# Optimization experiments

Measured on AMD Instinct MI355X. Metric: run time of the kernel, lower is better.

The kernel has to match this reference:

```python
import jax, jax.numpy as jnp
import numpy as np

VLAD_K = 8   # vlad_cluster
GHOST_K = 2  # ghost_cluster
IN_DIM = 512
EPS = 1e-12  # F.normalize eps


def setup_inputs() -> dict:
    key = jax.random.key(0)
    k1, k2, k3, k4 = jax.random.split(key, 4)
    N, C, H, W = 32, IN_DIM, 16, 64
    KG = VLAD_K + GHOST_K
    x = jax.random.normal(k1, (N, C, H, W), dtype=jnp.float32)
    # 1x1 conv weight [KG, C, 1, 1] -> store as [KG, C]; bias [KG]
    conv_w = jax.random.normal(k2, (KG, C), dtype=jnp.float32) * (1.0 / np.sqrt(C))
    conv_b = jax.random.normal(k3, (KG,), dtype=jnp.float32) * 0.01
    centers = jax.random.uniform(k4, (KG, C), dtype=jnp.float32)
    return {"x": x, "conv_w": conv_w, "conv_b": conv_b, "centers": centers}


def reference(x, conv_w, conv_b, centers):
    N, C, H, W = x.shape
    P = H * W
    xf = x.reshape(N, C, P)                                   # [N,C,P]
    # 1x1 conv == per-position matmul over channels
    logits = jnp.einsum('ncp,kc->nkp', xf, conv_w) + conv_b[None, :, None]
    a = jax.nn.softmax(logits, axis=1)                        # softmax over clusters, [N,KG,P]
    # algebraic rewrite of sum_p a*(x - c): (a @ x^T) - (sum_p a) * c
    ax = jnp.einsum('nkp,ncp->nkc', a, xf)                    # [N,KG,C]
    a_sum = a.sum(axis=-1)                                    # [N,KG]
    cluster_res = ax - a_sum[..., None] * centers[None]       # [N,KG,C]
    cluster_res = cluster_res[:, :VLAD_K, :]                  # drop ghost clusters
    norm = jnp.linalg.norm(cluster_res, axis=-1, keepdims=True)
    cluster_res = cluster_res / jnp.maximum(norm, EPS)        # L2 normalize per cluster
    return cluster_res.reshape(N, VLAD_K * C)
```

## Files before the change

### kernel.cpp

```cpp
#include <hip/hip_runtime.h>
#include <math.h>

#define N_    32
#define C_    512
#define P_    1024
#define KG_   10
#define KV_   8
#define PBLK_ 64
#define NPB_  (P_ / PBLK_)
#define PS_   81

__global__ __launch_bounds__(512) void vlad_logits(
    const float* __restrict__ x, const float* __restrict__ w,
    const float* __restrict__ bias, float* __restrict__ a_ws,
    float* __restrict__ asum_blk) {
  __shared__ float part[PBLK_ * PS_];
  const int t  = threadIdx.x;
  const int pl = t & 63;
  const int cg = __builtin_amdgcn_readfirstlane(threadIdx.x >> 6);
  const int n  = blockIdx.x >> 4;
  const int pb = blockIdx.x & 15;
  const int p0 = pb * PBLK_;

  const float* xp = x + ((size_t)n * C_ + cg * 64) * P_ + p0 + pl;

  float acc[KG_];
#pragma unroll
  for (int k = 0; k < KG_; ++k) acc[k] = 0.f;

#pragma unroll 8
  for (int i = 0; i < 64; ++i) {
    const float xv = xp[(size_t)i * P_];
    const int c = cg * 64 + i;
#pragma unroll
    for (int k = 0; k < KG_; ++k) acc[k] += xv * w[k * C_ + c];
  }

#pragma unroll
  for (int k = 0; k < KG_; ++k) part[pl * PS_ + cg * KG_ + k] = acc[k];
  __syncthreads();

  if (t < 64) {
    float l[KG_];
    float m = -1e30f;
#pragma unroll
    for (int k = 0; k < KG_; ++k) {
      float s = bias[k];
#pragma unroll
      for (int g = 0; g < 8; ++g) s += part[t * PS_ + g * KG_ + k];
      l[k] = s;
      m = fmaxf(m, s);
    }
    float sum = 0.f;
#pragma unroll
    for (int k = 0; k < KG_; ++k) { l[k] = __expf(l[k] - m); sum += l[k]; }
    const float inv = 1.f / sum;
#pragma unroll
    for (int k = 0; k < KV_; ++k) {
      const float a = l[k] * inv;
      a_ws[((size_t)n * KV_ + k) * P_ + p0 + t] = a;
      float s = a;
      s += __shfl_xor(s, 1, 64);  s += __shfl_xor(s, 2, 64);
      s += __shfl_xor(s, 4, 64);  s += __shfl_xor(s, 8, 64);
      s += __shfl_xor(s, 16, 64); s += __shfl_xor(s, 32, 64);
      if (t == 0) asum_blk[(n * NPB_ + pb) * KV_ + k] = s;
    }
  }
}

__global__ __launch_bounds__(256) void vlad_ax(
    const float* __restrict__ x, const float* __restrict__ a_ws,
    float* __restrict__ ax_ws) {
  const int n    = blockIdx.x >> 5;
  const int cb   = blockIdx.x & 31;
  const int lane = threadIdx.x & 63;
  const int wv   = threadIdx.x >> 6;
  const int c0   = cb * 16 + wv * 4;

  const float* ap = a_ws + (size_t)n * KV_ * P_;
  const float* xp = x + (size_t)n * C_ * P_;

  float acc[4][8];
#pragma unroll
  for (int cc = 0; cc < 4; ++cc)
#pragma unroll
    for (int k = 0; k < 8; ++k) acc[cc][k] = 0.f;

#pragma unroll
  for (int i = 0; i < 4; ++i) {
    const int pb = i * 256 + lane * 4;
    float4 a4[8];
#pragma unroll
    for (int k = 0; k < 8; ++k)
      a4[k] = *reinterpret_cast<const float4*>(ap + (size_t)k * P_ + pb);
#pragma unroll
    for (int cc = 0; cc < 4; ++cc) {
      float4 x4 = *reinterpret_cast<const float4*>(xp + (size_t)(c0 + cc) * P_ + pb);
#pragma unroll
      for (int k = 0; k < 8; ++k)
        acc[cc][k] += x4.x * a4[k].x + x4.y * a4[k].y
                    + x4.z * a4[k].z + x4.w * a4[k].w;
    }
  }

  float v[32];
#pragma unroll
  for (int cc = 0; cc < 4; ++cc)
#pragma unroll
    for (int k = 0; k < 8; ++k) v[cc * 8 + k] = acc[cc][k];

  {
    const bool hi = lane & 1;
#pragma unroll
    for (int j = 0; j < 16; ++j) {
      float send = hi ? v[j] : v[j + 16];
      float keep = hi ? v[j + 16] : v[j];
      v[j] = keep + __shfl_xor(send, 1, 64);
    }
  }
  {
    const bool hi = lane & 2;
#pragma unroll
    for (int j = 0; j < 8; ++j) {
      float send = hi ? v[j] : v[j + 8];
      float keep = hi ? v[j + 8] : v[j];
      v[j] = keep + __shfl_xor(send, 2, 64);
    }
  }
  {
    const bool hi = lane & 4;
#pragma unroll
    for (int j = 0; j < 4; ++j) {
      float send = hi ? v[j] : v[j + 4];
      float keep = hi ? v[j + 4] : v[j];
      v[j] = keep + __shfl_xor(send, 4, 64);
    }
  }
  {
    const bool hi = lane & 8;
#pragma unroll
    for (int j = 0; j < 2; ++j) {
      float send = hi ? v[j] : v[j + 2];
      float keep = hi ? v[j + 2] : v[j];
      v[j] = keep + __shfl_xor(send, 8, 64);
    }
  }
  {
    const bool hi = lane & 16;
    float send = hi ? v[0] : v[1];
    float keep = hi ? v[1] : v[0];
    v[0] = keep + __shfl_xor(send, 16, 64);
  }
  v[0] += __shfl_xor(v[0], 32, 64);

  if (lane < 32) {
    const int o = ((lane & 1) << 4) | ((lane & 2) << 2) | (lane & 4)
                | (((lane >> 3) & 1) << 1) | ((lane >> 4) & 1);
    const int cc = o >> 3;
    const int k  = o & 7;
    ax_ws[((size_t)n * KV_ + k) * C_ + (c0 + cc)] = v[0];
  }
}

__global__ __launch_bounds__(256) void vlad_fin(
    const float* __restrict__ ax_ws, const float* __restrict__ asum_blk,
    const float* __restrict__ centers, float* __restrict__ out) {
  __shared__ float sred[4];
  const int n = blockIdx.x >> 3;
  const int k = blockIdx.x & 7;
  const int t = threadIdx.x, lane = t & 63, wv = t >> 6;

  float asv = 0.f;
#pragma unroll
  for (int pb = 0; pb < NPB_; ++pb)
    asv += asum_blk[(n * NPB_ + pb) * KV_ + k];

  const int c = t * 2;
  const float2 av = *reinterpret_cast<const float2*>(&ax_ws[((size_t)n * KV_ + k) * C_ + c]);
  const float2 ct = *reinterpret_cast<const float2*>(&centers[k * C_ + c]);
  const float r0 = av.x - asv * ct.x;
  const float r1 = av.y - asv * ct.y;

  float ss = r0 * r0 + r1 * r1;
#pragma unroll
  for (int d = 1; d < 64; d <<= 1) ss += __shfl_xor(ss, d, 64);
  if (lane == 0) sred[wv] = ss;
  __syncthreads();
  const float tot = (sred[0] + sred[1]) + (sred[2] + sred[3]);
  const float inv = 1.f / fmaxf(sqrtf(tot), 1e-12f);

  out[(size_t)n * (KV_ * C_) + k * C_ + c]     = r0 * inv;
  out[(size_t)n * (KV_ * C_) + k * C_ + c + 1] = r1 * inv;
}

extern "C" void kernel_launch(void* const* d_in, const int* in_sizes, int n_in,
                              void* d_out, int out_size, void* d_ws, size_t ws_size,
                              hipStream_t stream) {
  const float* x       = (const float*)d_in[0];
  const float* conv_w  = (const float*)d_in[1];
  const float* conv_b  = (const float*)d_in[2];
  const float* centers = (const float*)d_in[3];
  float* out = (float*)d_out;

  float* a_ws     = (float*)d_ws;
  float* ax_ws    = a_ws + (size_t)N_ * KV_ * P_;
  float* asum_blk = ax_ws + (size_t)N_ * KV_ * C_;

  hipLaunchKernelGGL(vlad_logits, dim3(N_ * NPB_), dim3(512), 0, stream,
                     x, conv_w, conv_b, a_ws, asum_blk);
  hipLaunchKernelGGL(vlad_ax,     dim3(N_ * 32),   dim3(256), 0, stream,
                     x, a_ws, ax_ws);
  hipLaunchKernelGGL(vlad_fin,    dim3(N_ * KV_),  dim3(256), 0, stream,
                     ax_ws, asum_blk, centers, out);
}
```

Before: 116.2 us.

## Split channel and position reductions across more blocks with separate softmax kernel

The logits kernel now splits the channel reduction into two halves per position block, doubling the grid to 1024 blocks and writing partial logits to workspace. A new small softmax kernel combines the two partials, applies bias and softmax, and produces the assignments and per-block sums. The ax kernel likewise splits positions into two halves for twice as many blocks, and the final kernel adds the two partial ax results. The aim is more parallelism on a GPU with many CUs, at the cost of an extra kernel launch and extra workspace traffic.

```diff
diff --git a/kernel.cpp b/kernel.cpp
--- a/kernel.cpp
+++ b/kernel.cpp
@@ -10,75 +10,95 @@
 #define NPB_  (P_ / PBLK_)
 #define PS_   81
 
-__global__ __launch_bounds__(512) void vlad_logits(
+__global__ __launch_bounds__(512, 8) void vlad_logits_p(
     const float* __restrict__ x, const float* __restrict__ w,
-    const float* __restrict__ bias, float* __restrict__ a_ws,
-    float* __restrict__ asum_blk) {
+    float* __restrict__ plg) {
   __shared__ float part[PBLK_ * PS_];
   const int t  = threadIdx.x;
   const int pl = t & 63;
-  const int cg = __builtin_amdgcn_readfirstlane(threadIdx.x >> 6);
+  const int cg = __builtin_amdgcn_readfirstlane(t >> 6);
+  const int bx = blockIdx.x;
+  const int n  = bx >> 5;
+  const int pb = (bx >> 1) & 15;
+  const int ch = bx & 1;
+  const int p0 = pb * PBLK_;
+  const int c0 = ch * 256 + cg * 32;
+
+  const float* xp = x + ((size_t)n * C_ + c0) * P_ + p0 + pl;
+  const float* wp = w + c0;
+
+  float acc[KG_];
+#pragma unroll
+  for (int k = 0; k < KG_; ++k) acc[k] = 0.f;
+
+#pragma unroll 8
+  for (int i = 0; i < 32; ++i) {
+    const float xv = xp[(size_t)i * P_];
+#pragma unroll
+    for (int k = 0; k < KG_; ++k) acc[k] += xv * wp[k * C_ + i];
+  }
+
+#pragma unroll
+  for (int k = 0; k < KG_; ++k) part[pl * PS_ + cg * KG_ + k] = acc[k];
+  __syncthreads();
+
+  if (t < 64) {
+    const size_t row = (size_t)((n * NPB_ + pb) * 2 + ch) * KG_ * 64;
+#pragma unroll
+    for (int k = 0; k < KG_; ++k) {
+      float s = 0.f;
+#pragma unroll
+      for (int g = 0; g < 8; ++g) s += part[t * PS_ + g * KG_ + k];
+      plg[row + k * 64 + t] = s;
+    }
+  }
+}
+
+__global__ __launch_bounds__(64) void vlad_softmax2(
+    const float* __restrict__ plg, const float* __restrict__ bias,
+    float* __restrict__ a_ws, float* __restrict__ asum_blk) {
+  const int t  = threadIdx.x;
   const int n  = blockIdx.x >> 4;
   const int pb = blockIdx.x & 15;
-  const int p0 = pb * PBLK_;
-
-  const float* xp = x + ((size_t)n * C_ + cg * 64) * P_ + p0 + pl;
-
-  float acc[KG_];
-#pragma unroll
-  for (int k = 0; k < KG_; ++k) acc[k] = 0.f;
-
-#pragma unroll 8
-  for (int i = 0; i < 64; ++i) {
-    const float xv = xp[(size_t)i * P_];
-    const int c = cg * 64 + i;
-#pragma unroll
-    for (int k = 0; k < KG_; ++k) acc[k] += xv * w[k * C_ + c];
-  }
-
-#pragma unroll
-  for (int k = 0; k < KG_; ++k) part[pl * PS_ + cg * KG_ + k] = acc[k];
-  __syncthreads();
-
-  if (t < 64) {
-    float l[KG_];
-    float m = -1e30f;
-#pragma unroll
-    for (int k = 0; k < KG_; ++k) {
-      float s = bias[k];
-#pragma unroll
-      for (int g = 0; g < 8; ++g) s += part[t * PS_ + g * KG_ + k];
-      l[k] = s;
-      m = fmaxf(m, s);
-    }
-    float sum = 0.f;
-#pragma unroll
-    for (int k = 0; k < KG_; ++k) { l[k] = __expf(l[k] - m); sum += l[k]; }
-    const float inv = 1.f / sum;
-#pragma unroll
-    for (int k = 0; k < KV_; ++k) {
-      const float a = l[k] * inv;
-      a_ws[((size_t)n * KV_ + k) * P_ + p0 + t] = a;
-      float s = a;
-      s += __shfl_xor(s, 1, 64);  s += __shfl_xor(s, 2, 64);
-      s += __shfl_xor(s, 4, 64);  s += __shfl_xor(s, 8, 64);
-      s += __shfl_xor(s, 16, 64); s += __shfl_xor(s, 32, 64);
-      if (t == 0) asum_blk[(n * NPB_ + pb) * KV_ + k] = s;
-    }
-  }
-}
-
-__global__ __launch_bounds__(256) void vlad_ax(
+  const size_t r0 = (size_t)((n * NPB_ + pb) * 2 + 0) * KG_ * 64;
+  const size_t r1 = (size_t)((n * NPB_ + pb) * 2 + 1) * KG_ * 64;
+
+  float l[KG_];
+  float m = -1e30f;
+#pragma unroll
+  for (int k = 0; k < KG_; ++k) {
+    l[k] = plg[r0 + k * 64 + t] + plg[r1 + k * 64 + t] + bias[k];
+    m = fmaxf(m, l[k]);
+  }
+  float sum = 0.f;
+#pragma unroll
+  for (int k = 0; k < KG_; ++k) { l[k] = __expf(l[k] - m); sum += l[k]; }
+  const float inv = 1.f / sum;
+#pragma unroll
+  for (int k = 0; k < KV_; ++k) {
+    const float a = l[k] * inv;
+    a_ws[((size_t)n * KV_ + k) * P_ + pb * PBLK_ + t] = a;
+    float s = a;
+    s += __shfl_xor(s, 1, 64);  s += __shfl_xor(s, 2, 64);
+    s += __shfl_xor(s, 4, 64);  s += __shfl_xor(s, 8, 64);
+    s += __shfl_xor(s, 16, 64); s += __shfl_xor(s, 32, 64);
+    if (t == 0) asum_blk[(n * NPB_ + pb) * KV_ + k] = s;
+  }
+}
+
+__global__ __launch_bounds__(256) void vlad_ax2(
     const float* __restrict__ x, const float* __restrict__ a_ws,
-    float* __restrict__ ax_ws) {
-  const int n    = blockIdx.x >> 5;
-  const int cb   = blockIdx.x & 31;
+    float* __restrict__ axp) {
+  const int bx   = blockIdx.x;
+  const int n    = bx >> 6;
+  const int cb   = (bx >> 1) & 31;
+  const int ph   = bx & 1;
   const int lane = threadIdx.x & 63;
   const int wv   = threadIdx.x >> 6;
   const int c0   = cb * 16 + wv * 4;
 
-  const float* ap = a_ws + (size_t)n * KV_ * P_;
-  const float* xp = x + (size_t)n * C_ * P_;
+  const float* ap = a_ws + (size_t)n * KV_ * P_ + ph * 512;
+  const float* xp = x + (size_t)n * C_ * P_ + ph * 512;
 
   float acc[4][8];
 #pragma unroll
@@ -87,7 +107,7 @@
     for (int k = 0; k < 8; ++k) acc[cc][k] = 0.f;
 
 #pragma unroll
-  for (int i = 0; i < 4; ++i) {
+  for (int i = 0; i < 2; ++i) {
     const int pb = i * 256 + lane * 4;
     float4 a4[8];
 #pragma unroll
@@ -109,44 +129,35 @@
 #pragma unroll
     for (int k = 0; k < 8; ++k) v[cc * 8 + k] = acc[cc][k];
 
-  {
-    const bool hi = lane & 1;
+  {  const bool hi = lane & 1;
 #pragma unroll
     for (int j = 0; j < 16; ++j) {
       float send = hi ? v[j] : v[j + 16];
       float keep = hi ? v[j + 16] : v[j];
       v[j] = keep + __shfl_xor(send, 1, 64);
-    }
-  }
-  {
-    const bool hi = lane & 2;
+    } }
+  {  const bool hi = lane & 2;
 #pragma unroll
     for (int j = 0; j < 8; ++j) {
       float send = hi ? v[j] : v[j + 8];
       float keep = hi ? v[j + 8] : v[j];
       v[j] = keep + __shfl_xor(send, 2, 64);
-    }
-  }
-  {
-    const bool hi = lane & 4;
+    } }
+  {  const bool hi = lane & 4;
 #pragma unroll
     for (int j = 0; j < 4; ++j) {
       float send = hi ? v[j] : v[j + 4];
       float keep = hi ? v[j + 4] : v[j];
       v[j] = keep + __shfl_xor(send, 4, 64);
-    }
-  }
-  {
-    const bool hi = lane & 8;
+    } }
+  {  const bool hi = lane & 8;
 #pragma unroll
     for (int j = 0; j < 2; ++j) {
       float send = hi ? v[j] : v[j + 2];
       float keep = hi ? v[j + 2] : v[j];
       v[j] = keep + __shfl_xor(send, 8, 64);
-    }
-  }
-  {
-    const bool hi = lane & 16;
+    } }
+  {  const bool hi = lane & 16;
     float send = hi ? v[0] : v[1];
     float keep = hi ? v[1] : v[0];
     v[0] = keep + __shfl_xor(send, 16, 64);
@@ -158,12 +169,12 @@
                 | (((lane >> 3) & 1) << 1) | ((lane >> 4) & 1);
     const int cc = o >> 3;
     const int k  = o & 7;
-    ax_ws[((size_t)n * KV_ + k) * C_ + (c0 + cc)] = v[0];
+    axp[((size_t)(n * 2 + ph) * KV_ + k) * C_ + (c0 + cc)] = v[0];
   }
 }
 
 __global__ __launch_bounds__(256) void vlad_fin(
-    const float* __restrict__ ax_ws, const float* __restrict__ asum_blk,
+    const float* __restrict__ axp, const float* __restrict__ asum_blk,
     const float* __restrict__ centers, float* __restrict__ out) {
   __shared__ float sred[4];
   const int n = blockIdx.x >> 3;
@@ -176,10 +187,13 @@
     asv += asum_blk[(n * NPB_ + pb) * KV_ + k];
 
   const int c = t * 2;
-  const float2 av = *reinterpret_cast<const float2*>(&ax_ws[((size_t)n * KV_ + k) * C_ + c]);
+  const float2 a0 = *reinterpret_cast<const float2*>(
+      &axp[((size_t)(n * 2 + 0) * KV_ + k) * C_ + c]);
+  const float2 a1 = *reinterpret_cast<const float2*>(
+      &axp[((size_t)(n * 2 + 1) * KV_ + k) * C_ + c]);
   const float2 ct = *reinterpret_cast<const float2*>(&centers[k * C_ + c]);
-  const float r0 = av.x - asv * ct.x;
-  const float r1 = av.y - asv * ct.y;
+  const float r0 = (a0.x + a1.x) - asv * ct.x;
+  const float r1 = (a0.y + a1.y) - asv * ct.y;
 
   float ss = r0 * r0 + r1 * r1;
 #pragma unroll
@@ -202,14 +216,17 @@
   const float* centers = (const float*)d_in[3];
   float* out = (float*)d_out;
 
-  float* a_ws     = (float*)d_ws;
-  float* ax_ws    = a_ws + (size_t)N_ * KV_ * P_;
-  float* asum_blk = ax_ws + (size_t)N_ * KV_ * C_;
-
-  hipLaunchKernelGGL(vlad_logits, dim3(N_ * NPB_), dim3(512), 0, stream,
-                     x, conv_w, conv_b, a_ws, asum_blk);
-  hipLaunchKernelGGL(vlad_ax,     dim3(N_ * 32),   dim3(256), 0, stream,
-                     x, a_ws, ax_ws);
-  hipLaunchKernelGGL(vlad_fin,    dim3(N_ * KV_),  dim3(256), 0, stream,
-                     ax_ws, asum_blk, centers, out);
-}
+  float* plg      = (float*)d_ws;
+  float* a_ws     = plg + (size_t)N_ * NPB_ * 2 * KG_ * 64;
+  float* axp      = a_ws + (size_t)N_ * KV_ * P_;
+  float* asum_blk = axp + (size_t)2 * N_ * KV_ * C_;
+
+  hipLaunchKernelGGL(vlad_logits_p, dim3(N_ * 32), dim3(512), 0, stream,
+                     x, conv_w, plg);
+  hipLaunchKernelGGL(vlad_softmax2, dim3(N_ * NPB_), dim3(64), 0, stream,
+                     plg, conv_b, a_ws, asum_blk);
+  hipLaunchKernelGGL(vlad_ax2,     dim3(N_ * 64), dim3(256), 0, stream,
+                     x, a_ws, axp);
+  hipLaunchKernelGGL(vlad_fin,     dim3(N_ * KV_), dim3(256), 0, stream,
+                     axp, asum_blk, centers, out);
+}
```

After: 125.6 us. 8.1% more time.

## Fuse logits/softmax and a·x into one kernel, reusing register-held x tile

Applied to the files above, without the earlier changes.

Merges the logits+softmax kernel and the a·x contraction kernel so each block loads its 64-position x slice into registers once and reuses it for both the conv logits and the weighted sum. Assignments go through shared memory instead of global workspace, and per-block partial a·x results are written out and summed across position blocks in the final kernel. This removes the second full read of x and one launch. In exchange it holds 64 floats per thread in registers, spends many cross-lane shuffles per channel, and writes a 16x larger partial buffer that the finalize kernel must reduce.

```diff
diff --git a/kernel.cpp b/kernel.cpp
--- a/kernel.cpp
+++ b/kernel.cpp
@@ -9,35 +9,40 @@
 #define PBLK_ 64
 #define NPB_  (P_ / PBLK_)
 #define PS_   81
+#define AS_   72
+#define XAS_  521
 
-__global__ __launch_bounds__(512) void vlad_logits(
+__global__ __launch_bounds__(512, 4) void vlad_main(
     const float* __restrict__ x, const float* __restrict__ w,
-    const float* __restrict__ bias, float* __restrict__ a_ws,
-    float* __restrict__ asum_blk) {
+    const float* __restrict__ bias,
+    float* __restrict__ part_ax, float* __restrict__ asum_blk) {
   __shared__ float part[PBLK_ * PS_];
-  const int t  = threadIdx.x;
-  const int pl = t & 63;
-  const int cg = __builtin_amdgcn_readfirstlane(threadIdx.x >> 6);
-  const int n  = blockIdx.x >> 4;
-  const int pb = blockIdx.x & 15;
-  const int p0 = pb * PBLK_;
+  __shared__ float a_l[KV_ * AS_];
+  __shared__ float sm_ax[KV_ * XAS_];
 
-  const float* xp = x + ((size_t)n * C_ + cg * 64) * P_ + p0 + pl;
+  const int t    = threadIdx.x;
+  const int lane = t & 63;
+  const int cg   = __builtin_amdgcn_readfirstlane(t >> 6);
+  const int n    = blockIdx.x >> 4;
+  const int pb   = blockIdx.x & 15;
+  const int p0   = pb * PBLK_;
+  const int c0   = cg * 64;
+
+  const float* xp = x + ((size_t)n * C_ + c0) * P_ + p0 + lane;
+  float xv[64];
+#pragma unroll
+  for (int i = 0; i < 64; ++i) xv[i] = xp[(size_t)i * P_];
 
   float acc[KG_];
 #pragma unroll
   for (int k = 0; k < KG_; ++k) acc[k] = 0.f;
-
-#pragma unroll 8
+#pragma unroll
   for (int i = 0; i < 64; ++i) {
-    const float xv = xp[(size_t)i * P_];
-    const int c = cg * 64 + i;
 #pragma unroll
-    for (int k = 0; k < KG_; ++k) acc[k] += xv * w[k * C_ + c];
+    for (int k = 0; k < KG_; ++k) acc[k] += xv[i] * w[k * C_ + c0 + i];
   }
-
 #pragma unroll
-  for (int k = 0; k < KG_; ++k) part[pl * PS_ + cg * KG_ + k] = acc[k];
+  for (int k = 0; k < KG_; ++k) part[lane * PS_ + cg * KG_ + k] = acc[k];
   __syncthreads();
 
   if (t < 64) {
@@ -58,7 +63,7 @@
 #pragma unroll
     for (int k = 0; k < KV_; ++k) {
       const float a = l[k] * inv;
-      a_ws[((size_t)n * KV_ + k) * P_ + p0 + t] = a;
+      a_l[k * AS_ + t] = a;
       float s = a;
       s += __shfl_xor(s, 1, 64);  s += __shfl_xor(s, 2, 64);
       s += __shfl_xor(s, 4, 64);  s += __shfl_xor(s, 8, 64);
@@ -66,104 +71,62 @@
       if (t == 0) asum_blk[(n * NPB_ + pb) * KV_ + k] = s;
     }
   }
-}
+  __syncthreads();
 
-__global__ __launch_bounds__(256) void vlad_ax(
-    const float* __restrict__ x, const float* __restrict__ a_ws,
-    float* __restrict__ ax_ws) {
-  const int n    = blockIdx.x >> 5;
-  const int cb   = blockIdx.x & 31;
-  const int lane = threadIdx.x & 63;
-  const int wv   = threadIdx.x >> 6;
-  const int c0   = cb * 16 + wv * 4;
+  float ak[KV_];
+#pragma unroll
+  for (int k = 0; k < KV_; ++k) ak[k] = a_l[k * AS_ + lane];
 
-  const float* ap = a_ws + (size_t)n * KV_ * P_;
-  const float* xp = x + (size_t)n * C_ * P_;
+  const int kmap = ((lane & 1) << 2) | (lane & 2) | ((lane >> 2) & 1);
 
-  float acc[4][8];
+#pragma unroll 8
+  for (int i = 0; i < 64; ++i) {
+    float v[KV_];
 #pragma unroll
-  for (int cc = 0; cc < 4; ++cc)
+    for (int k = 0; k < KV_; ++k) v[k] = ak[k] * xv[i];
+    {
+      const bool hi = lane & 1;
 #pragma unroll
-    for (int k = 0; k < 8; ++k) acc[cc][k] = 0.f;
+      for (int j = 0; j < 4; ++j) {
+        float send = hi ? v[j] : v[j + 4];
+        float keep = hi ? v[j + 4] : v[j];
+        v[j] = keep + __shfl_xor(send, 1, 64);
+      }
+    }
+    {
+      const bool hi = lane & 2;
+#pragma unroll
+      for (int j = 0; j < 2; ++j) {
+        float send = hi ? v[j] : v[j + 2];
+        float keep = hi ? v[j + 2] : v[j];
+        v[j] = keep + __shfl_xor(send, 2, 64);
+      }
+    }
+    {
+      const bool hi = lane & 4;
+      float send = hi ? v[0] : v[1];
+      float keep = hi ? v[1] : v[0];
+      v[0] = keep + __shfl_xor(send, 4, 64);
+    }
+    v[0] += __shfl_xor(v[0], 8, 64);
+    v[0] += __shfl_xor(v[0], 16, 64);
+    v[0] += __shfl_xor(v[0], 32, 64);
+    if (lane < 8) sm_ax[kmap * XAS_ + c0 + i] = v[0];
+  }
+  __syncthreads();
 
+  const size_t base = (size_t)(n * NPB_ + pb) * KV_ * C_;
 #pragma unroll
-  for (int i = 0; i < 4; ++i) {
-    const int pb = i * 256 + lane * 4;
-    float4 a4[8];
-#pragma unroll
-    for (int k = 0; k < 8; ++k)
-      a4[k] = *reinterpret_cast<const float4*>(ap + (size_t)k * P_ + pb);
-#pragma unroll
-    for (int cc = 0; cc < 4; ++cc) {
-      float4 x4 = *reinterpret_cast<const float4*>(xp + (size_t)(c0 + cc) * P_ + pb);
-#pragma unroll
-      for (int k = 0; k < 8; ++k)
-        acc[cc][k] += x4.x * a4[k].x + x4.y * a4[k].y
-                    + x4.z * a4[k].z + x4.w * a4[k].w;
-    }
-  }
-
-  float v[32];
-#pragma unroll
-  for (int cc = 0; cc < 4; ++cc)
-#pragma unroll
-    for (int k = 0; k < 8; ++k) v[cc * 8 + k] = acc[cc][k];
-
-  {
-    const bool hi = lane & 1;
-#pragma unroll
-    for (int j = 0; j < 16; ++j) {
-      float send = hi ? v[j] : v[j + 16];
-      float keep = hi ? v[j + 16] : v[j];
-      v[j] = keep + __shfl_xor(send, 1, 64);
-    }
-  }
-  {
-    const bool hi = lane & 2;
-#pragma unroll
-    for (int j = 0; j < 8; ++j) {
-      float send = hi ? v[j] : v[j + 8];
-      float keep = hi ? v[j + 8] : v[j];
-      v[j] = keep + __shfl_xor(send, 2, 64);
-    }
-  }
-  {
-    const bool hi = lane & 4;
-#pragma unroll
-    for (int j = 0; j < 4; ++j) {
-      float send = hi ? v[j] : v[j + 4];
-      float keep = hi ? v[j + 4] : v[j];
-      v[j] = keep + __shfl_xor(send, 4, 64);
-    }
-  }
-  {
-    const bool hi = lane & 8;
-#pragma unroll
-    for (int j = 0; j < 2; ++j) {
-      float send = hi ? v[j] : v[j + 2];
-      float keep = hi ? v[j + 2] : v[j];
-      v[j] = keep + __shfl_xor(send, 8, 64);
-    }
-  }
-  {
-    const bool hi = lane & 16;
-    float send = hi ? v[0] : v[1];
-    float keep = hi ? v[1] : v[0];
-    v[0] = keep + __shfl_xor(send, 16, 64);
-  }
-  v[0] += __shfl_xor(v[0], 32, 64);
-
-  if (lane < 32) {
-    const int o = ((lane & 1) << 4) | ((lane & 2) << 2) | (lane & 4)
-                | (((lane >> 3) & 1) << 1) | ((lane >> 4) & 1);
-    const int cc = o >> 3;
-    const int k  = o & 7;
-    ax_ws[((size_t)n * KV_ + k) * C_ + (c0 + cc)] = v[0];
+  for (int r = 0; r < 8; ++r) {
+    const int idx = r * 512 + t;
+    const int k = idx >> 9;
+    const int c = idx & 511;
+    part_ax[base + idx] = sm_ax[k * XAS_ + c];
   }
 }
 
 __global__ __launch_bounds__(256) void vlad_fin(
-    const float* __restrict__ ax_ws, const float* __restrict__ asum_blk,
+    const float* __restrict__ part_ax, const float* __restrict__ asum_blk,
     const float* __restrict__ centers, float* __restrict__ out) {
   __shared__ float sred[4];
   const int n = blockIdx.x >> 3;
@@ -176,10 +139,16 @@
     asv += asum_blk[(n * NPB_ + pb) * KV_ + k];
 
   const int c = t * 2;
-  const float2 av = *reinterpret_cast<const float2*>(&ax_ws[((size_t)n * KV_ + k) * C_ + c]);
+  float s0 = 0.f, s1 = 0.f;
+#pragma unroll
+  for (int pb = 0; pb < NPB_; ++pb) {
+    const float2 v = *reinterpret_cast<const float2*>(
+        &part_ax[((size_t)(n * NPB_ + pb) * KV_ + k) * C_ + c]);
+    s0 += v.x; s1 += v.y;
+  }
   const float2 ct = *reinterpret_cast<const float2*>(&centers[k * C_ + c]);
-  const float r0 = av.x - asv * ct.x;
-  const float r1 = av.y - asv * ct.y;
+  const float r0 = s0 - asv * ct.x;
+  const float r1 = s1 - asv * ct.y;
 
   float ss = r0 * r0 + r1 * r1;
 #pragma unroll
@@ -189,8 +158,10 @@
   const float tot = (sred[0] + sred[1]) + (sred[2] + sred[3]);
   const float inv = 1.f / fmaxf(sqrtf(tot), 1e-12f);
 
-  out[(size_t)n * (KV_ * C_) + k * C_ + c]     = r0 * inv;
-  out[(size_t)n * (KV_ * C_) + k * C_ + c + 1] = r1 * inv;
+  float2 o;
+  o.x = r0 * inv;
+  o.y = r1 * inv;
+  *reinterpret_cast<float2*>(&out[(size_t)n * (KV_ * C_) + k * C_ + c]) = o;
 }
 
 extern "C" void kernel_launch(void* const* d_in, const int* in_sizes, int n_in,
@@ -202,14 +173,11 @@
   const float* centers = (const float*)d_in[3];
   float* out = (float*)d_out;
 
-  float* a_ws     = (float*)d_ws;
-  float* ax_ws    = a_ws + (size_t)N_ * KV_ * P_;
-  float* asum_blk = ax_ws + (size_t)N_ * KV_ * C_;
+  float* part_ax  = (float*)d_ws;
+  float* asum_blk = part_ax + (size_t)N_ * NPB_ * KV_ * C_;
 
-  hipLaunchKernelGGL(vlad_logits, dim3(N_ * NPB_), dim3(512), 0, stream,
-                     x, conv_w, conv_b, a_ws, asum_blk);
-  hipLaunchKernelGGL(vlad_ax,     dim3(N_ * 32),   dim3(256), 0, stream,
-                     x, a_ws, ax_ws);
-  hipLaunchKernelGGL(vlad_fin,    dim3(N_ * KV_),  dim3(256), 0, stream,
-                     ax_ws, asum_blk, centers, out);
+  hipLaunchKernelGGL(vlad_main, dim3(N_ * NPB_), dim3(512), 0, stream,
+                     x, conv_w, conv_b, part_ax, asum_blk);
+  hipLaunchKernelGGL(vlad_fin,  dim3(N_ * KV_),  dim3(256), 0, stream,
+                     part_ax, asum_blk, centers, out);
 }
```

After: 163.3 us. 40.5% more time.
